# Optimization experiments

Measured on AMD Instinct MI355X. Metric: run time of the kernel, lower is better.

The kernel has to match this reference:

```python
import jax, jax.numpy as jnp
import numpy as np

COMMITMENT_COST = 0.25
EPS = 1e-10


def setup_inputs() -> dict:
    key = jax.random.key(0)
    k1, k2 = jax.random.split(key)
    B, C, H, W = 16, 64, 128, 128          # C == embedding_dim
    K, D = 512, 64                          # codebook size, embedding_dim
    inputs = jax.random.normal(k1, (B, C, H, W), dtype=jnp.float32)
    # nn.Embedding init: uniform(-1/K, 1/K)
    embedding = jax.random.uniform(k2, (K, D), dtype=jnp.float32,
                                   minval=-1.0 / K, maxval=1.0 / K)
    return {"inputs": inputs, "embedding": embedding}


def reference(inputs, embedding):
    # NCHW -> NHWC, flatten to tokens [N, D]
    x = jnp.transpose(inputs, (0, 2, 3, 1))
    nhwc_shape = x.shape
    flat = x.reshape(-1, embedding.shape[1])                       # [N, D]

    distances = (jnp.sum(flat * flat, axis=1, keepdims=True)
                 + jnp.sum(embedding * embedding, axis=1)
                 - 2.0 * flat @ embedding.T)
    idx = jnp.argmin(distances, axis=1)                            # [N]

    # one-hot encodings (returned), quantized via direct gather
    encodings = jax.nn.one_hot(idx, embedding.shape[0], dtype=flat.dtype)  # [N, K]
    quantized = embedding[idx].reshape(nhwc_shape)                 # [B,H,W,D]

    e_latent = jnp.mean((jax.lax.stop_gradient(quantized) - x) ** 2)
    q_latent = jnp.mean((quantized - jax.lax.stop_gradient(x)) ** 2)
    loss = q_latent + COMMITMENT_COST * e_latent

    # straight-through estimator
    quantized_st = x + jax.lax.stop_gradient(quantized - x)

    avg_probs = jnp.mean(encodings, axis=0)                        # [K]
    perplexity = jnp.exp(-jnp.sum(avg_probs * jnp.log(avg_probs + EPS)))

    return (loss, jnp.transpose(quantized_st, (0, 3, 1, 2)), perplexity, encodings)
```

## Files before the change

### kernel.cpp

```cpp
#include <hip/hip_runtime.h>
#include <math.h>


#define NTOK    262144
#define KCODES  512
#define DDIM    64
#define CSTRIDE 16384
#define IMG     1048576
#define QOFF    1
#define POFF    16777217
#define EOFF    16777218
#define EBF     8192
#define SUBFLT  32768

typedef short bf16x8 __attribute__((ext_vector_type(8)));
typedef float f32x4  __attribute__((ext_vector_type(4)));

__device__ __forceinline__ unsigned short f2bf(float f) {
    unsigned u = __float_as_uint(f);
    return (unsigned short)((u + 0x7fffu + ((u >> 16) & 1u)) >> 16);
}

__device__ __forceinline__ float np_pairwise_sq64(const float* v) {
    float r[8];
#pragma unroll
    for (int j = 0; j < 8; ++j) r[j] = __fmul_rn(v[j], v[j]);
#pragma unroll
    for (int i = 8; i < 64; i += 8) {
#pragma unroll
        for (int j = 0; j < 8; ++j)
            r[j] = __fadd_rn(r[j], __fmul_rn(v[i + j], v[i + j]));
    }
    float s01 = __fadd_rn(r[0], r[1]);
    float s23 = __fadd_rn(r[2], r[3]);
    float s45 = __fadd_rn(r[4], r[5]);
    float s67 = __fadd_rn(r[6], r[7]);
    return __fadd_rn(__fadd_rn(s01, s23), __fadd_rn(s45, s67));
}

__global__ __launch_bounds__(256) void vq_prep(const float* __restrict__ emb,
                                               float* __restrict__ ws) {
    const int tid = threadIdx.x, blk = blockIdx.x;
    if (blk < 8) {
        unsigned short* ebf = (unsigned short*)(ws + EBF);
#pragma unroll
        for (int ii = 0; ii < 16; ++ii) {
            int t = blk * 4096 + ii * 256 + tid;
            ebf[t] = f2bf(emb[t]);
        }
    } else {
#pragma unroll
        for (int r = 0; r < 2; ++r) {
            const int k = tid * 2 + r;
            const float* e = emb + (size_t)k * DDIM;
            float v[64];
#pragma unroll
            for (int i = 0; i < 64; ++i) v[i] = e[i];
            ws[512 + k] = np_pairwise_sq64(v);
        }
    }
}

__global__ __launch_bounds__(256) void vq_main(const float* __restrict__ in,
                                               const float* __restrict__ emb,
                                               float* __restrict__ out,
                                               float* __restrict__ ws) {
    __shared__ float          xs[64 * 64];
    __shared__ unsigned short xbf[64 * 68];
    __shared__ float          bsh[512];
    __shared__ int            idx_sh[64];
    __shared__ float          red[4];

    const int tid = threadIdx.x, blk = blockIdx.x;
    const int T0 = blk * 64, b = T0 >> 14, hw0 = T0 & 16383;

    {
        const float4* gx = (const float4*)(in + (size_t)b * IMG + hw0);
        float4* xs4 = (float4*)xs;
#pragma unroll
        for (int jj = 0; jj < 4; ++jj) {
            int t = tid + jj * 256;
            int c = t >> 4, q = t & 15;
            xs4[t] = gx[(size_t)c * (CSTRIDE / 4) + q];
        }
    }
    bsh[tid]       = ws[512 + tid];
    bsh[256 + tid] = ws[768 + tid];
    __syncthreads();

    {
        const int t = tid & 63, d0 = (tid >> 6) * 16;
#pragma unroll
        for (int dd = 0; dd < 16; ++dd)
            xbf[t * 68 + d0 + dd] = f2bf(xs[(d0 + dd) * 64 + t]);
    }
    __syncthreads();

    const int l = tid & 63, w = tid >> 6;
    const int lm = l & 15, lg = l >> 4;

    const bf16x8 a0 = *(const bf16x8*)(xbf + (w * 16 + lm) * 68 + lg * 8);
    const bf16x8 a1 = *(const bf16x8*)(xbf + (w * 16 + lm) * 68 + 32 + lg * 8);

    const unsigned short* ebf = (const unsigned short*)(ws + EBF);
    const unsigned short* ep  = ebf + lm * 64 + lg * 8;

    float dmin[4]; int idx[4];
#pragma unroll
    for (int r = 0; r < 4; ++r) { dmin[r] = 3.402823466e38f; idx[r] = 0; }
    const f32x4 zero = {0.f, 0.f, 0.f, 0.f};

#pragma unroll 4
    for (int nt = 0; nt < 32; ++nt) {
        bf16x8 b0 = *(const bf16x8*)(ep + nt * 1024);
        bf16x8 b1 = *(const bf16x8*)(ep + nt * 1024 + 32);
        f32x4 acc = __builtin_amdgcn_mfma_f32_16x16x32_bf16(a0, b0, zero, 0, 0, 0);
        acc       = __builtin_amdgcn_mfma_f32_16x16x32_bf16(a1, b1, acc,  0, 0, 0);
        const int   code = nt * 16 + lm;
        const float bk   = bsh[code];
#pragma unroll
        for (int r = 0; r < 4; ++r) {
            float s = fmaf(-2.0f, acc[r], bk);
            if (s < dmin[r]) { dmin[r] = s; idx[r] = code; }
        }
    }

#pragma unroll
    for (int m = 1; m < 16; m <<= 1) {
#pragma unroll
        for (int r = 0; r < 4; ++r) {
            float od = __shfl_xor(dmin[r], m, 64);
            int   oi = __shfl_xor(idx[r],  m, 64);
            if (od < dmin[r] || (od == dmin[r] && oi < idx[r])) {
                dmin[r] = od; idx[r] = oi;
            }
        }
    }
    if (lm == 0) {
#pragma unroll
        for (int r = 0; r < 4; ++r) idx_sh[w * 16 + lg * 4 + r] = idx[r];
    }
    __syncthreads();

    const int tl = tid & 63, chh = (tid >> 6) * 16;
    const int id = idx_sh[tl];
    if (tid < 64) atomicAdd((int*)ws + id, 1);

    float*       q  = out + QOFF + (size_t)b * IMG + hw0 + tl;
    const float* e0 = emb + (size_t)id * DDIM + chh;

    float lsum = 0.f;
#pragma unroll
    for (int cc = 0; cc < 16; ++cc) {
        float x   = xs[(chh + cc) * 64 + tl];
        float dqx = __fsub_rn(e0[cc], x);
        lsum = __fadd_rn(lsum, __fmul_rn(dqx, dqx));
        q[(size_t)(chh + cc) * CSTRIDE] = __fadd_rn(x, dqx);
    }
#pragma unroll
    for (int off = 32; off > 0; off >>= 1) lsum += __shfl_down(lsum, off, 64);
    if ((tid & 63) == 0) red[tid >> 6] = lsum;
    __syncthreads();
    if (tid == 0) ws[1024 + blk] = red[0] + red[1] + red[2] + red[3];

    float4* s4 = (float4*)(out + EOFF + (size_t)blk * SUBFLT);
#pragma unroll 4
    for (int ii = 0; ii < 32; ++ii) {
        int jj = ii * 256 + tid;
        int ix = idx_sh[jj >> 7];
        int c0 = (jj & 127) << 2;
        float4 v;
        v.x = (c0     == ix) ? 1.0f : 0.0f;
        v.y = (c0 + 1 == ix) ? 1.0f : 0.0f;
        v.z = (c0 + 2 == ix) ? 1.0f : 0.0f;
        v.w = (c0 + 3 == ix) ? 1.0f : 0.0f;
        s4[jj] = v;
    }
}

__global__ void vq_final(float* __restrict__ out, const float* __restrict__ ws) {
    __shared__ float sl[512], sp[512];
    int t = threadIdx.x;
    float s = 0.f;
#pragma unroll
    for (int r = 0; r < 8; ++r) s += ws[1024 + t + 512 * r];
    sl[t] = s;
    int cnt = ((const int*)ws)[t];
    float p = (float)cnt * (1.0f / 262144.0f);
    sp[t] = p * logf(p + 1e-10f);
    __syncthreads();
    for (int off = 256; off > 0; off >>= 1) {
        if (t < off) { sl[t] += sl[t + off]; sp[t] += sp[t + off]; }
        __syncthreads();
    }
    if (t == 0) {
        float m = sl[0] * (1.0f / 16777216.0f);
        out[0]    = __fadd_rn(m, __fmul_rn(0.25f, m));
        out[POFF] = expf(-sp[0]);
    }
}

extern "C" void kernel_launch(void* const* d_in, const int* in_sizes, int n_in,
                              void* d_out, int out_size, void* d_ws, size_t ws_size,
                              hipStream_t stream) {
    const float* in  = (const float*)d_in[0];
    const float* emb = (const float*)d_in[1];
    float* out = (float*)d_out;
    float* ws  = (float*)d_ws;

    hipMemsetAsync(d_ws, 0, 512 * sizeof(int), stream);
    hipLaunchKernelGGL(vq_prep,  dim3(9),    dim3(256), 0, stream, emb, ws);
    hipLaunchKernelGGL(vq_main,  dim3(4096), dim3(256), 0, stream, in, emb, out, ws);
    hipLaunchKernelGGL(vq_final, dim3(1),    dim3(512), 0, stream, out, ws);
}
```

Before: 754.1 us.

## Zero one-hot output early with nontemporal stores and scatter ones afterwards

```diff
diff --git a/kernel.cpp b/kernel.cpp
--- a/kernel.cpp
+++ b/kernel.cpp
@@ -65,7 +65,6 @@
                                                const float* __restrict__ emb,
                                                float* __restrict__ out,
                                                float* __restrict__ ws) {
-    __shared__ float          xs[64 * 64];
     __shared__ unsigned short xbf[64 * 68];
     __shared__ float          bsh[512];
     __shared__ int            idx_sh[64];
@@ -74,26 +73,33 @@
     const int tid = threadIdx.x, blk = blockIdx.x;
     const int T0 = blk * 64, b = T0 >> 14, hw0 = T0 & 16383;
 
-    {
-        const float4* gx = (const float4*)(in + (size_t)b * IMG + hw0);
-        float4* xs4 = (float4*)xs;
-#pragma unroll
-        for (int jj = 0; jj < 4; ++jj) {
-            int t = tid + jj * 256;
-            int c = t >> 4, q = t & 15;
-            xs4[t] = gx[(size_t)c * (CSTRIDE / 4) + q];
-        }
-    }
-    bsh[tid]       = ws[512 + tid];
-    bsh[256 + tid] = ws[768 + tid];
-    __syncthreads();
-
-    {
-        const int t = tid & 63, d0 = (tid >> 6) * 16;
-#pragma unroll
-        for (int dd = 0; dd < 16; ++dd)
-            xbf[t * 68 + d0 + dd] = f2bf(xs[(d0 + dd) * 64 + t]);
-    }
+    const float4* gx = (const float4*)(in + (size_t)b * IMG + hw0);
+    float4 g[4];
+#pragma unroll
+    for (int jj = 0; jj < 4; ++jj) {
+        int t = tid + jj * 256;
+        g[jj] = gx[(size_t)(t >> 4) * (CSTRIDE / 4) + (t & 15)];
+    }
+    const float bk0 = ws[512 + tid];
+    const float bk1 = ws[768 + tid];
+
+    f32x4* sub4 = (f32x4*)(out + EOFF + (size_t)blk * SUBFLT);
+    const f32x4 z4 = {0.f, 0.f, 0.f, 0.f};
+#pragma unroll
+    for (int ii = 0; ii < 32; ++ii)
+        __builtin_nontemporal_store(z4, sub4 + ii * 256 + tid);
+
+#pragma unroll
+    for (int jj = 0; jj < 4; ++jj) {
+        int t = tid + jj * 256;
+        int c = t >> 4, q = (t & 15) * 4;
+        xbf[(q + 0) * 68 + c] = f2bf(g[jj].x);
+        xbf[(q + 1) * 68 + c] = f2bf(g[jj].y);
+        xbf[(q + 2) * 68 + c] = f2bf(g[jj].z);
+        xbf[(q + 3) * 68 + c] = f2bf(g[jj].w);
+    }
+    bsh[tid]       = bk0;
+    bsh[256 + tid] = bk1;
     __syncthreads();
 
     const int l = tid & 63, w = tid >> 6;
@@ -146,16 +152,18 @@
     const int id = idx_sh[tl];
     if (tid < 64) atomicAdd((int*)ws + id, 1);
 
+    const float* px = in  + (size_t)b * IMG + hw0 + tl;
     float*       q  = out + QOFF + (size_t)b * IMG + hw0 + tl;
     const float* e0 = emb + (size_t)id * DDIM + chh;
 
     float lsum = 0.f;
 #pragma unroll
     for (int cc = 0; cc < 16; ++cc) {
-        float x   = xs[(chh + cc) * 64 + tl];
+        float x   = px[(size_t)(chh + cc) * CSTRIDE];
         float dqx = __fsub_rn(e0[cc], x);
         lsum = __fadd_rn(lsum, __fmul_rn(dqx, dqx));
-        q[(size_t)(chh + cc) * CSTRIDE] = __fadd_rn(x, dqx);
+        __builtin_nontemporal_store(__fadd_rn(x, dqx),
+                                    q + (size_t)(chh + cc) * CSTRIDE);
     }
 #pragma unroll
     for (int off = 32; off > 0; off >>= 1) lsum += __shfl_down(lsum, off, 64);
@@ -163,18 +171,11 @@
     __syncthreads();
     if (tid == 0) ws[1024 + blk] = red[0] + red[1] + red[2] + red[3];
 
-    float4* s4 = (float4*)(out + EOFF + (size_t)blk * SUBFLT);
-#pragma unroll 4
-    for (int ii = 0; ii < 32; ++ii) {
-        int jj = ii * 256 + tid;
-        int ix = idx_sh[jj >> 7];
-        int c0 = (jj & 127) << 2;
-        float4 v;
-        v.x = (c0     == ix) ? 1.0f : 0.0f;
-        v.y = (c0 + 1 == ix) ? 1.0f : 0.0f;
-        v.z = (c0 + 2 == ix) ? 1.0f : 0.0f;
-        v.w = (c0 + 3 == ix) ? 1.0f : 0.0f;
-        s4[jj] = v;
+    if (tid < 64) {
+        const int ix = idx_sh[tid];
+        f32x4 v = {0.f, 0.f, 0.f, 0.f};
+        v[ix & 3] = 1.0f;
+        __builtin_nontemporal_store(v, sub4 + tid * 128 + (ix >> 2));
     }
 }
 
@@ -208,7 +209,7 @@
     float* out = (float*)d_out;
     float* ws  = (float*)d_ws;
 
-    hipMemsetAsync(d_ws, 0, 512 * sizeof(int), stream);
+    (void)hipMemsetAsync(d_ws, 0, 512 * sizeof(int), stream);
     hipLaunchKernelGGL(vq_prep,  dim3(9),    dim3(256), 0, stream, emb, ws);
     hipLaunchKernelGGL(vq_main,  dim3(4096), dim3(256), 0, stream, in, emb, out, ws);
     hipLaunchKernelGGL(vq_final, dim3(1),    dim3(512), 0, stream, out, ws);
```

New measurement: 728.1 us. 1.04x faster.
